# Optimization experiments

Measured on AMD Instinct MI355X. Metric: run time of the kernel, lower is better.

## Reference

```python
import jax, jax.numpy as jnp
import numpy as np

HEADS = 12
FEATURES = 768
D_HEAD = FEATURES // HEADS
SCALE = float(np.sqrt(D_HEAD))
EPS = 1e-12
N = 2048


def setup_inputs() -> dict:
    key = jax.random.key(0)
    ks = jax.random.split(key, 5)
    init = 1.0 / np.sqrt(FEATURES)
    return {
        "x": jax.random.normal(ks[0], (N, FEATURES), dtype=jnp.float32),
        "Wq": jax.random.normal(ks[1], (FEATURES, FEATURES), dtype=jnp.float32) * init,
        "Wk": jax.random.normal(ks[2], (FEATURES, FEATURES), dtype=jnp.float32) * init,
        "Wv": jax.random.normal(ks[3], (FEATURES, FEATURES), dtype=jnp.float32) * init,
        "Wo": jax.random.normal(ks[4], (FEATURES, FEATURES), dtype=jnp.float32) * init,
        "gamma": jnp.ones((FEATURES,), dtype=jnp.float32),
        "beta": jnp.zeros((FEATURES,), dtype=jnp.float32),
    }


def reference(x, Wq, Wk, Wv, Wo, gamma, beta):
    n = x.shape[0]
    # projections (no bias); weight layout [out, in] -> x @ W.T
    q = (x @ Wq.T).reshape(n, HEADS, D_HEAD).transpose(1, 0, 2)  # [h, n, d]
    k = (x @ Wk.T).reshape(n, HEADS, D_HEAD).transpose(1, 0, 2)
    v = (x @ Wv.T).reshape(n, HEADS, D_HEAD).transpose(1, 0, 2)
    # scores [h, n, n]; original divides q@k^T by sqrt(d_head)
    att = jnp.einsum("hnd,hmd->hnm", q, k) / SCALE
    att = jax.nn.softmax(att, axis=-1)  # dropout p=0 -> identity
    out = jnp.einsum("hnm,hmd->hnd", att, v)  # [h, n, d]
    out = out.transpose(1, 0, 2).reshape(n, FEATURES)  # n (h d)
    out = out @ Wo.T
    # residual + layernorm (eps=1e-12)
    y = out + x
    mu = jnp.mean(y, axis=-1, keepdims=True)
    var = jnp.mean((y - mu) ** 2, axis=-1, keepdims=True)
    return (y - mu) / jnp.sqrt(var + EPS) * gamma + beta
```

## Files before the change

kernel.cpp:

```cpp
#include <hip/hip_runtime.h>
#include <hip/hip_bf16.h>
#include <math.h>

#define N_TOK 2048
#define FEAT  768
#define HEADS 12
#define DHEAD 64
#define SPLIT 4
#define KV_PER (N_TOK / SPLIT)

typedef __bf16 v8bf __attribute__((ext_vector_type(8)));
typedef __bf16 v4bf __attribute__((ext_vector_type(4)));
typedef float  v4f  __attribute__((ext_vector_type(4)));

#define XE ((size_t)N_TOK * FEAT)
#define WE ((size_t)FEAT * FEAT)
#define QK_LD 1536

#define SCALE_FOLD 0.18033688011112042f

__device__ __forceinline__ void gload16(const __bf16* g, __bf16* l) {
    __builtin_amdgcn_global_load_lds(
        (const __attribute__((address_space(1))) unsigned int*)g,
        (__attribute__((address_space(3))) unsigned int*)l, 16, 0, 0);
}

__global__ __launch_bounds__(256) void cvt_all(
        const float* __restrict__ x,  const float* __restrict__ Wq,
        const float* __restrict__ Wk, const float* __restrict__ Wv,
        const float* __restrict__ Wo,
        __bf16* __restrict__ xb, __bf16* __restrict__ wqkv, __bf16* __restrict__ wob) {
    size_t i = ((size_t)blockIdx.x * 256 + threadIdx.x) * 4;
    const float* src; __bf16* dst; size_t off; float scale = 1.f;
    if (i < XE)               { src = x;  dst = xb;          off = i; }
    else if (i < XE + WE)     { src = Wq; dst = wqkv;        off = i - XE; scale = SCALE_FOLD; }
    else if (i < XE + 2 * WE) { src = Wk; dst = wqkv + WE;   off = i - XE - WE; }
    else if (i < XE + 3 * WE) { src = Wv; dst = wqkv + 2*WE; off = i - XE - 2*WE; }
    else                      { src = Wo; dst = wob;         off = i - XE - 3*WE; }
    float4 v = *(const float4*)(src + off);
    v4bf o;
    o[0] = (__bf16)(v.x * scale); o[1] = (__bf16)(v.y * scale);
    o[2] = (__bf16)(v.z * scale); o[3] = (__bf16)(v.w * scale);
    *(v4bf*)(dst + off) = o;
}

__global__ __launch_bounds__(256) void gemm_qkv(
        const __bf16* __restrict__ A, const __bf16* __restrict__ B,
        __bf16* __restrict__ qk, __bf16* __restrict__ vt) {
    __shared__ __bf16 As[64][64];
    __shared__ __bf16 Bs[128][64];
    const int t    = threadIdx.x;
    const int lane = t & 63, w = t >> 6;
    const int quad = lane >> 4, l15 = lane & 15;
    const int wm = w & 1, wn = w >> 1;
    const int bm = blockIdx.y * 64, bn = blockIdx.x * 128;
    const int lr8 = lane >> 3;
    const int gs  = ((lane & 7) ^ lr8) * 8;

    v4f acc[2][4] = {};
    for (int k0 = 0; k0 < FEAT; k0 += 64) {
        gload16(A + (size_t)(bm + w * 16 +      lr8) * FEAT + k0 + gs, &As[w * 16][0]);
        gload16(A + (size_t)(bm + w * 16 + 8 +  lr8) * FEAT + k0 + gs, &As[w * 16 + 8][0]);
        gload16(B + (size_t)(bn + w * 32 +      lr8) * FEAT + k0 + gs, &Bs[w * 32][0]);
        gload16(B + (size_t)(bn + w * 32 + 8 +  lr8) * FEAT + k0 + gs, &Bs[w * 32 + 8][0]);
        gload16(B + (size_t)(bn + w * 32 + 16 + lr8) * FEAT + k0 + gs, &Bs[w * 32 + 16][0]);
        gload16(B + (size_t)(bn + w * 32 + 24 + lr8) * FEAT + k0 + gs, &Bs[w * 32 + 24][0]);
        __syncthreads();
#pragma unroll
        for (int kk = 0; kk < 2; kk++) {
            const int fo = ((kk * 4 + quad) ^ (l15 & 7)) * 8;
            v8bf a[2], b[4];
#pragma unroll
            for (int mi = 0; mi < 2; mi++) a[mi] = *(const v8bf*)&As[wm * 32 + mi * 16 + l15][fo];
#pragma unroll
            for (int ni = 0; ni < 4; ni++) b[ni] = *(const v8bf*)&Bs[wn * 64 + ni * 16 + l15][fo];
#pragma unroll
            for (int mi = 0; mi < 2; mi++)
#pragma unroll
                for (int ni = 0; ni < 4; ni++)
                    acc[mi][ni] = __builtin_amdgcn_mfma_f32_16x16x32_bf16(a[mi], b[ni], acc[mi][ni], 0, 0, 0);
        }
        __syncthreads();
    }
    if (bn < 2 * FEAT) {
#pragma unroll
        for (int mi = 0; mi < 2; mi++)
#pragma unroll
            for (int ni = 0; ni < 4; ni++) {
                int col = bn + wn * 64 + ni * 16 + l15;
#pragma unroll
                for (int r = 0; r < 4; r++) {
                    int row = bm + wm * 32 + mi * 16 + quad * 4 + r;
                    qk[(size_t)row * QK_LD + col] = (__bf16)acc[mi][ni][r];
                }
            }
    } else {
#pragma unroll
        for (int mi = 0; mi < 2; mi++)
#pragma unroll
            for (int ni = 0; ni < 4; ni++) {
                int col = bn + wn * 64 + ni * 16 + l15 - 2 * FEAT;
                int row = bm + wm * 32 + mi * 16 + quad * 4;
                v4bf pk;
#pragma unroll
                for (int r = 0; r < 4; r++) pk[r] = (__bf16)acc[mi][ni][r];
                *(v4bf*)(vt + (size_t)col * N_TOK + row) = pk;
            }
    }
}

__global__ __launch_bounds__(256, 4) void attention(
        const __bf16* __restrict__ QK, const __bf16* __restrict__ vt,
        __bf16* __restrict__ Opart, float* __restrict__ lpart) {
    __shared__ __bf16 KV[2][2][64][64];
    __shared__ __bf16 PT[4][32][32];
    const int t    = threadIdx.x;
    const int lane = t & 63, w = t >> 6;
    const int quad = lane >> 4, l15 = lane & 15;
    const int h = blockIdx.y, s = blockIdx.z;
    const int q0 = blockIdx.x * 128 + w * 32;
    const int sw3 = l15 & 3;

    v8bf qf[2][2];
#pragma unroll
    for (int qt = 0; qt < 2; qt++) {
        const __bf16* qp = QK + (size_t)(q0 + qt * 16 + l15) * QK_LD + h * DHEAD + quad * 8;
        qf[qt][0] = *(const v8bf*)qp;
        qf[qt][1] = *(const v8bf*)(qp + 32);
    }
    const __bf16* kg = QK + FEAT + h * DHEAD;
    const __bf16* vg = vt + (size_t)(h * DHEAD) * N_TOK;

    v4f o_acc[4][2] = {};
    float lacc[2] = {0.f, 0.f};

    const int kvbeg = s * KV_PER;
    const int lr8 = lane >> 3;

    auto stage = [&](int b, int kv0) {
#pragma unroll
        for (int i = 0; i < 2; i++) {
            int row = w * 16 + i * 8 + lr8;
            int gsk = (lane & 7) ^ (row & 7);
            gload16(kg + (size_t)(kv0 + row) * QK_LD + gsk * 8, &KV[b][0][w * 16 + i * 8][0]);
            gload16(vg + (size_t)row * N_TOK + kv0 + gsk * 8,   &KV[b][1][w * 16 + i * 8][0]);
        }
    };

    auto step = [&](int b) {
#pragma unroll
        for (int half = 0; half < 2; half++) {
#pragma unroll
            for (int kk = 0; kk < 2; kk++) {
                int kvt = half * 2 + kk;
                v8bf kf0 = *(const v8bf*)&KV[b][0][kvt * 16 + l15][((0 + quad) ^ (l15 & 7)) * 8];
                v8bf kf1 = *(const v8bf*)&KV[b][0][kvt * 16 + l15][((4 + quad) ^ (l15 & 7)) * 8];
                const int wcol = ((kk * 2 + (quad >> 1)) ^ sw3) * 8 + (quad & 1) * 4;
#pragma unroll
                for (int qt = 0; qt < 2; qt++) {
                    v4f a = {};
                    a = __builtin_amdgcn_mfma_f32_16x16x32_bf16(kf0, qf[qt][0], a, 0, 0, 0);
                    a = __builtin_amdgcn_mfma_f32_16x16x32_bf16(kf1, qf[qt][1], a, 0, 0, 0);
                    float p0 = __builtin_amdgcn_exp2f(a[0]);
                    float p1 = __builtin_amdgcn_exp2f(a[1]);
                    float p2 = __builtin_amdgcn_exp2f(a[2]);
                    float p3 = __builtin_amdgcn_exp2f(a[3]);
                    lacc[qt] += (p0 + p1) + (p2 + p3);
                    v4bf pk;
                    pk[0] = (__bf16)p0; pk[1] = (__bf16)p1; pk[2] = (__bf16)p2; pk[3] = (__bf16)p3;
                    *(v4bf*)&PT[w][qt * 16 + l15][wcol] = pk;
                }
            }
            v8bf vf[4], ptf[2];
#pragma unroll
            for (int dt = 0; dt < 4; dt++)
                vf[dt] = *(const v8bf*)&KV[b][1][dt * 16 + l15][((half * 4 + quad) ^ (l15 & 7)) * 8];
#pragma unroll
            for (int qt = 0; qt < 2; qt++)
                ptf[qt] = *(const v8bf*)&PT[w][qt * 16 + l15][(quad ^ sw3) * 8];
#pragma unroll
            for (int dt = 0; dt < 4; dt++)
#pragma unroll
                for (int qt = 0; qt < 2; qt++)
                    o_acc[dt][qt] = __builtin_amdgcn_mfma_f32_16x16x32_bf16(vf[dt], ptf[qt], o_acc[dt][qt], 0, 0, 0);
        }
    };

    stage(0, kvbeg);
    const int TILES = KV_PER / 64;
    for (int tt = 0; tt < TILES; tt++) {
        __syncthreads();
        if (tt + 1 < TILES) stage((tt + 1) & 1, kvbeg + (tt + 1) * 64);
        step(tt & 1);
    }

    __bf16* op = Opart + (size_t)s * XE;
#pragma unroll
    for (int qt = 0; qt < 2; qt++) {
        float l = lacc[qt];
        l += __shfl_xor(l, 16); l += __shfl_xor(l, 32);
        float linv = 1.0f / l;
        int q = q0 + qt * 16 + l15;
        if (quad == 0) lpart[((size_t)s * HEADS + h) * N_TOK + q] = l;
#pragma unroll
        for (int dt = 0; dt < 4; dt++) {
            v4bf pk;
#pragma unroll
            for (int r = 0; r < 4; r++) pk[r] = (__bf16)(o_acc[dt][qt][r] * linv);
            *(v4bf*)(op + (size_t)q * FEAT + h * DHEAD + dt * 16 + quad * 4) = pk;
        }
    }
}

__global__ __launch_bounds__(256) void combine(
        const __bf16* __restrict__ Op, const float* __restrict__ lp, __bf16* __restrict__ Ob) {
    size_t i = ((size_t)blockIdx.x * 256 + threadIdx.x) * 4;
    int row = (int)(i / FEAT), col = (int)(i % FEAT), h = col >> 6;
    float ls[SPLIT], tot = 0.f;
#pragma unroll
    for (int s = 0; s < SPLIT; s++) {
        ls[s] = lp[((size_t)s * HEADS + h) * N_TOK + row];
        tot += ls[s];
    }
    float inv = 1.0f / tot;
    float a0 = 0.f, a1 = 0.f, a2 = 0.f, a3 = 0.f;
#pragma unroll
    for (int s = 0; s < SPLIT; s++) {
        v4bf p = *(const v4bf*)(Op + s * XE + i);
        float wgt = ls[s] * inv;
        a0 += wgt * (float)p[0]; a1 += wgt * (float)p[1];
        a2 += wgt * (float)p[2]; a3 += wgt * (float)p[3];
    }
    v4bf o;
    o[0] = (__bf16)a0; o[1] = (__bf16)a1; o[2] = (__bf16)a2; o[3] = (__bf16)a3;
    *(v4bf*)(Ob + i) = o;
}

__global__ __launch_bounds__(256) void gemm_out(
        const __bf16* __restrict__ Ob, const __bf16* __restrict__ Wo,
        const float* __restrict__ x, float* __restrict__ Yf) {
    __shared__ __bf16 As[64][32];
    __shared__ __bf16 Bs[128][32];
    const int t    = threadIdx.x;
    const int lane = t & 63, w = t >> 6;
    const int quad = lane >> 4, l15 = lane & 15;
    const int wm = w & 1, wn = w >> 1;
    const int bm = blockIdx.y * 64, bn = blockIdx.x * 128;
    const int srow = lane >> 2, scol = (lane & 3) * 8;

    v4f acc[2][4] = {};
    for (int k0 = 0; k0 < FEAT; k0 += 32) {
        gload16(Ob + (size_t)(bm + w * 16 + srow) * FEAT + k0 + scol,      &As[w * 16][0]);
        gload16(Wo + (size_t)(bn + w * 32 + srow) * FEAT + k0 + scol,      &Bs[w * 32][0]);
        gload16(Wo + (size_t)(bn + w * 32 + 16 + srow) * FEAT + k0 + scol, &Bs[w * 32 + 16][0]);
        __syncthreads();
        v8bf a[2], b[4];
#pragma unroll
        for (int mi = 0; mi < 2; mi++) a[mi] = *(const v8bf*)&As[wm * 32 + mi * 16 + l15][quad * 8];
#pragma unroll
        for (int ni = 0; ni < 4; ni++) b[ni] = *(const v8bf*)&Bs[wn * 64 + ni * 16 + l15][quad * 8];
#pragma unroll
        for (int mi = 0; mi < 2; mi++)
#pragma unroll
            for (int ni = 0; ni < 4; ni++)
                acc[mi][ni] = __builtin_amdgcn_mfma_f32_16x16x32_bf16(a[mi], b[ni], acc[mi][ni], 0, 0, 0);
        __syncthreads();
    }
#pragma unroll
    for (int mi = 0; mi < 2; mi++)
#pragma unroll
        for (int ni = 0; ni < 4; ni++) {
            int col = bn + wn * 64 + ni * 16 + l15;
#pragma unroll
            for (int r = 0; r < 4; r++) {
                int row = bm + wm * 32 + mi * 16 + quad * 4 + r;
                Yf[(size_t)row * FEAT + col] = acc[mi][ni][r] + x[(size_t)row * FEAT + col];
            }
        }
}

__global__ __launch_bounds__(256) void ln_kernel(
        const float* __restrict__ Y, const float* __restrict__ gamma,
        const float* __restrict__ beta, float* __restrict__ out) {
    __shared__ float sbuf[4];
    const int row = blockIdx.x, t = threadIdx.x;
    const float* y = Y + (size_t)row * FEAT;
    float v0 = y[t], v1 = y[t + 256], v2 = y[t + 512];
    float s = v0 + v1 + v2;
#pragma unroll
    for (int m = 32; m; m >>= 1) s += __shfl_xor(s, m);
    if ((t & 63) == 0) sbuf[t >> 6] = s;
    __syncthreads();
    float mean = (sbuf[0] + sbuf[1] + sbuf[2] + sbuf[3]) * (1.f / FEAT);
    __syncthreads();
    float d0 = v0 - mean, d1 = v1 - mean, d2 = v2 - mean;
    float q = d0 * d0 + d1 * d1 + d2 * d2;
#pragma unroll
    for (int m = 32; m; m >>= 1) q += __shfl_xor(q, m);
    if ((t & 63) == 0) sbuf[t >> 6] = q;
    __syncthreads();
    float var = (sbuf[0] + sbuf[1] + sbuf[2] + sbuf[3]) * (1.f / FEAT);
    float rs = rsqrtf(var + 1e-12f);
    float* o = out + (size_t)row * FEAT;
    o[t]       = d0 * rs * gamma[t]       + beta[t];
    o[t + 256] = d1 * rs * gamma[t + 256] + beta[t + 256];
    o[t + 512] = d2 * rs * gamma[t + 512] + beta[t + 512];
}

extern "C" void kernel_launch(void* const* d_in, const int* in_sizes, int n_in,
                              void* d_out, int out_size, void* d_ws, size_t ws_size,
                              hipStream_t stream) {
    const float* x     = (const float*)d_in[0];
    const float* Wq    = (const float*)d_in[1];
    const float* Wk    = (const float*)d_in[2];
    const float* Wv    = (const float*)d_in[3];
    const float* Wo    = (const float*)d_in[4];
    const float* gamma = (const float*)d_in[5];
    const float* beta  = (const float*)d_in[6];
    float* out = (float*)d_out;

    char* ws = (char*)d_ws;
    size_t off = 0;
    auto alloc = [&](size_t bytes) -> void* {
        void* p = ws + off;
        off += (bytes + 255) & ~(size_t)255;
        return p;
    };
    __bf16* xb   = (__bf16*)alloc(XE * 2);
    __bf16* wqkv = (__bf16*)alloc(3 * WE * 2);
    __bf16* wob  = (__bf16*)alloc(WE * 2);
    __bf16* qk   = (__bf16*)alloc((size_t)N_TOK * QK_LD * 2);
    __bf16* vtb  = (__bf16*)alloc((size_t)FEAT * N_TOK * 2);
    __bf16* Op   = (__bf16*)alloc(SPLIT * XE * 2);
    float*  lp   = (float*)alloc(SPLIT * HEADS * N_TOK * 4);
    __bf16* Ob   = vtb;
    float*  Yf   = (float*)ws;

    cvt_all<<<(int)((XE + 4 * WE) / 4 / 256), 256, 0, stream>>>(x, Wq, Wk, Wv, Wo, xb, wqkv, wob);

    gemm_qkv<<<dim3((QK_LD + FEAT) / 128, N_TOK / 64), 256, 0, stream>>>(xb, wqkv, qk, vtb);

    attention<<<dim3(N_TOK / 128, HEADS, SPLIT), 256, 0, stream>>>(qk, vtb, Op, lp);

    combine<<<(int)(XE / 4 / 256), 256, 0, stream>>>(Op, lp, Ob);

    gemm_out<<<dim3(FEAT / 128, N_TOK / 64), 256, 0, stream>>>(Ob, wob, x, Yf);

    ln_kernel<<<N_TOK, 256, 0, stream>>>(Yf, gamma, beta, out);
}
```

Baseline: 135.9 us.

## Load K fragments directly from global into registers, stage only V in LDS

The attention kernel now reads K tiles straight from global memory into register fragments, double-buffered across two register sets, and stages only V through LDS. This halves LDS use and removes the LDS round-trip and reads for K. The cost is more VGPRs and duplicated global K reads across the four waves, so occupancy is lowered to three blocks per SIMD in launch bounds. The loop is manually unrolled by two to alternate between the register buffers.

```diff
diff --git a/kernel.cpp b/kernel.cpp
--- a/kernel.cpp
+++ b/kernel.cpp
@@ -109,10 +109,10 @@
     }
 }
 
-__global__ __launch_bounds__(256, 4) void attention(
+__global__ __launch_bounds__(256, 3) void attention(
         const __bf16* __restrict__ QK, const __bf16* __restrict__ vt,
         __bf16* __restrict__ Opart, float* __restrict__ lpart) {
-    __shared__ __bf16 KV[2][2][64][64];
+    __shared__ __bf16 KV[2][64][64];
     __shared__ __bf16 PT[4][32][32];
     const int t    = threadIdx.x;
     const int lane = t & 63, w = t >> 6;
@@ -128,39 +128,44 @@
         qf[qt][0] = *(const v8bf*)qp;
         qf[qt][1] = *(const v8bf*)(qp + 32);
     }
-    const __bf16* kg = QK + FEAT + h * DHEAD;
+    const __bf16* kg = QK + FEAT + h * DHEAD + quad * 8;
     const __bf16* vg = vt + (size_t)(h * DHEAD) * N_TOK;
 
     v4f o_acc[4][2] = {};
     float lacc[2] = {0.f, 0.f};
 
-    const int kvbeg = s * KV_PER;
+    const int kvbeg = s * KV_PER, kvend = kvbeg + KV_PER;
     const int lr8 = lane >> 3;
 
-    auto stage = [&](int b, int kv0) {
+    auto stage_v = [&](int b, int kv0) {
 #pragma unroll
         for (int i = 0; i < 2; i++) {
             int row = w * 16 + i * 8 + lr8;
             int gsk = (lane & 7) ^ (row & 7);
-            gload16(kg + (size_t)(kv0 + row) * QK_LD + gsk * 8, &KV[b][0][w * 16 + i * 8][0]);
-            gload16(vg + (size_t)row * N_TOK + kv0 + gsk * 8,   &KV[b][1][w * 16 + i * 8][0]);
+            gload16(vg + (size_t)row * N_TOK + kv0 + gsk * 8, &KV[b][w * 16 + i * 8][0]);
         }
     };
-
-    auto step = [&](int b) {
+    auto load_k = [&](int kv0, v8bf kf[4][2]) {
+#pragma unroll
+        for (int kvt = 0; kvt < 4; kvt++) {
+            const __bf16* kp = kg + (size_t)(kv0 + kvt * 16 + l15) * QK_LD;
+            kf[kvt][0] = *(const v8bf*)kp;
+            kf[kvt][1] = *(const v8bf*)(kp + 32);
+        }
+    };
+
+    auto step = [&](int b, v8bf kf[4][2]) {
 #pragma unroll
         for (int half = 0; half < 2; half++) {
 #pragma unroll
             for (int kk = 0; kk < 2; kk++) {
                 int kvt = half * 2 + kk;
-                v8bf kf0 = *(const v8bf*)&KV[b][0][kvt * 16 + l15][((0 + quad) ^ (l15 & 7)) * 8];
-                v8bf kf1 = *(const v8bf*)&KV[b][0][kvt * 16 + l15][((4 + quad) ^ (l15 & 7)) * 8];
                 const int wcol = ((kk * 2 + (quad >> 1)) ^ sw3) * 8 + (quad & 1) * 4;
 #pragma unroll
                 for (int qt = 0; qt < 2; qt++) {
                     v4f a = {};
-                    a = __builtin_amdgcn_mfma_f32_16x16x32_bf16(kf0, qf[qt][0], a, 0, 0, 0);
-                    a = __builtin_amdgcn_mfma_f32_16x16x32_bf16(kf1, qf[qt][1], a, 0, 0, 0);
+                    a = __builtin_amdgcn_mfma_f32_16x16x32_bf16(kf[kvt][0], qf[qt][0], a, 0, 0, 0);
+                    a = __builtin_amdgcn_mfma_f32_16x16x32_bf16(kf[kvt][1], qf[qt][1], a, 0, 0, 0);
                     float p0 = __builtin_amdgcn_exp2f(a[0]);
                     float p1 = __builtin_amdgcn_exp2f(a[1]);
                     float p2 = __builtin_amdgcn_exp2f(a[2]);
@@ -174,7 +179,7 @@
             v8bf vf[4], ptf[2];
 #pragma unroll
             for (int dt = 0; dt < 4; dt++)
-                vf[dt] = *(const v8bf*)&KV[b][1][dt * 16 + l15][((half * 4 + quad) ^ (l15 & 7)) * 8];
+                vf[dt] = *(const v8bf*)&KV[b][dt * 16 + l15][((half * 4 + quad) ^ (l15 & 7)) * 8];
 #pragma unroll
             for (int qt = 0; qt < 2; qt++)
                 ptf[qt] = *(const v8bf*)&PT[w][qt * 16 + l15][(quad ^ sw3) * 8];
@@ -186,12 +191,16 @@
         }
     };
 
-    stage(0, kvbeg);
-    const int TILES = KV_PER / 64;
-    for (int tt = 0; tt < TILES; tt++) {
-        __syncthreads();
-        if (tt + 1 < TILES) stage((tt + 1) & 1, kvbeg + (tt + 1) * 64);
-        step(tt & 1);
+    v8bf kfA[4][2], kfB[4][2];
+    stage_v(0, kvbeg);
+    load_k(kvbeg, kfA);
+    for (int kv0 = kvbeg; kv0 < kvend; kv0 += 128) {
+        __syncthreads();
+        if (kv0 + 64 < kvend) { stage_v(1, kv0 + 64); load_k(kv0 + 64, kfB); }
+        step(0, kfA);
+        __syncthreads();
+        if (kv0 + 128 < kvend) { stage_v(0, kv0 + 128); load_k(kv0 + 128, kfA); }
+        step(1, kfB);
     }
 
     __bf16* op = Opart + (size_t)s * XE;
```

Result: slower. 171.1 us (+25.9%).
